# Kernel optimization log

Measured on AMD Instinct MI355X. Metric: run time of the kernel, lower is better.

The kernel has to match this reference:

```python
import jax, jax.numpy as jnp
import numpy as np

FP4_E2M1_VALUES = [0.0, 0.0625, 8.0, 1.0, 2.0, 3.0, 4.0, 6.0,
                   -0.0, -0.0625, -8.0, -1.0, -2.0, -3.0, -4.0, -6.0]

M, N, K = 4096, 4096, 4096


def setup_inputs() -> dict:
    key = jax.random.key(0)
    k1, k2 = jax.random.split(key)
    x = jax.random.normal(k1, (M, K), dtype=jnp.float16)
    # packed uint8 bytes stored as int32 (values in [0,256)); each byte holds
    # two fp4 indices: high nibble = even k, low nibble = odd k
    packed_weight = jax.random.randint(k2, (N, K // 2), 0, 256, dtype=jnp.int32)
    lut = jnp.array(FP4_E2M1_VALUES, dtype=jnp.float16)
    return {"x": x, "packed_weight": packed_weight, "lut": lut}


def reference(x, packed_weight, lut):
    # Dequantize: unpack nibbles along K, LUT lookup -> W [N, K] fp16
    n, kh = packed_weight.shape
    high = (packed_weight >> 4) & 15   # even k positions
    low = packed_weight & 15           # odd k positions
    idx = jnp.stack([high, low], axis=-1).reshape(n, 2 * kh)  # [N, K]
    w = lut[idx]                       # [N, K] fp16
    # GEMM with fp32 accumulation (Triton kernel accumulates in fp32), cast to fp16
    y = jnp.einsum('mk,nk->mn', x, w, preferred_element_type=jnp.float32)
    return y.astype(jnp.float16)
```

## Files before the change

### kernel.cpp

```cpp
#include <hip/hip_runtime.h>
#include <hip/hip_fp16.h>
#include <stdint.h>

#define M_DIM 4096
#define N_DIM 4096
#define K_DIM 4096
#define KW (K_DIM / 2)
#define WS_XH_BYTES ((size_t)M_DIM * K_DIM * 2)
#define WS_WH_BYTES ((size_t)N_DIM * K_DIM * 2)

typedef _Float16 half8 __attribute__((ext_vector_type(8)));
typedef float f32x4 __attribute__((ext_vector_type(4)));

__device__ __forceinline__ uint32_t pk2(float a, float b) {
  auto h = __builtin_amdgcn_cvt_pkrtz(a, b);
  return __builtin_bit_cast(uint32_t, h);
}

__device__ __forceinline__ uint32_t dq(uint32_t b, uint32_t ph, uint32_t pl) {
#if __has_builtin(__builtin_amdgcn_perm)
  const uint32_t sel = ((b & 0x70u) << 4) | ((b & 0x07u) << 24);
  uint32_t v = __builtin_amdgcn_perm(ph, pl, sel);
#else
  const uint64_t pool = ((uint64_t)ph << 32) | pl;
  const uint32_t mh = (uint32_t)(pool >> (((b >> 4) & 7u) * 8)) & 0xFFu;
  const uint32_t ml = (uint32_t)(pool >> ((b & 7u) * 8)) & 0xFFu;
  uint32_t v = (mh << 8) | (ml << 24);
#endif
  const uint32_t sg = ((b & 0x88u) * 0x10000100u) & 0x80008000u;
  return v | sg;
}

__device__ __forceinline__ void lut_pool(const float* __restrict__ lutf,
                                         uint32_t& ph, uint32_t& pl) {
  const uint32_t h01 = pk2(lutf[0], lutf[1]);
  const uint32_t h23 = pk2(lutf[2], lutf[3]);
  const uint32_t h45 = pk2(lutf[4], lutf[5]);
  const uint32_t h67 = pk2(lutf[6], lutf[7]);
#if __has_builtin(__builtin_amdgcn_perm)
  pl = __builtin_amdgcn_perm(h23, h01, 0x07050301u);
  ph = __builtin_amdgcn_perm(h67, h45, 0x07050301u);
#else
  pl = ((h01 >> 8) & 0xFFu) | ((h01 >> 24) << 8) |
       (((h23 >> 8) & 0xFFu) << 16) | ((h23 >> 24) << 24);
  ph = ((h45 >> 8) & 0xFFu) | ((h45 >> 24) << 8) |
       (((h67 >> 8) & 0xFFu) << 16) | ((h67 >> 24) << 24);
#endif
}

#define XBLOCKS (M_DIM * K_DIM / 8 / 256)
#define WBLOCKS (N_DIM * KW / 4 / 256)

__global__ __launch_bounds__(256) void prep_kernel(
    const float4* __restrict__ xin, uint4* __restrict__ xout,
    const int4* __restrict__ pin, uint4* __restrict__ wout,
    const float* __restrict__ lutf) {
  const int b = blockIdx.x;
  if (b < XBLOCKS) {
    const int i = b * 256 + threadIdx.x;
    const float4 v0 = xin[2 * i];
    const float4 v1 = xin[2 * i + 1];
    xout[i] = make_uint4(pk2(v0.x, v0.y), pk2(v0.z, v0.w),
                         pk2(v1.x, v1.y), pk2(v1.z, v1.w));
  } else {
    uint32_t ph, pl;
    lut_pool(lutf, ph, pl);
    const int i = (b - XBLOCKS) * 256 + threadIdx.x;
    const int4 w = pin[i];
    wout[i] = make_uint4(dq(w.x, ph, pl), dq(w.y, ph, pl),
                         dq(w.z, ph, pl), dq(w.w, ph, pl));
  }
}

__global__ __launch_bounds__(256) void cvt_x_kernel(const float4* __restrict__ xin,
                                                    uint4* __restrict__ xout) {
  const int i = blockIdx.x * 256 + threadIdx.x;
  const float4 v0 = xin[2 * i];
  const float4 v1 = xin[2 * i + 1];
  xout[i] = make_uint4(pk2(v0.x, v0.y), pk2(v0.z, v0.w),
                       pk2(v1.x, v1.y), pk2(v1.z, v1.w));
}

__device__ __forceinline__ f32x4 mfma16(half8 a, half8 b, f32x4 c) {
  return __builtin_amdgcn_mfma_f32_16x16x32_f16(a, b, c, 0, 0, 0);
}

#define NT (K_DIM / 64)
#define SGB __builtin_amdgcn_sched_group_barrier
#define SG_MFMA 0x8
#define SG_VMEM 0x10
#define SG_DSRD 0x100

__global__ __launch_bounds__(512, 2) void f16gemm256_kernel(
    const uint8_t* __restrict__ xh,
    const uint8_t* __restrict__ wh,
    float* __restrict__ out)
{
  __shared__ uint16_t Al[2][2][256 * 32];
  __shared__ uint16_t Bl[2][2][256 * 32];

  const int tid  = threadIdx.x;
  const int lane = tid & 63;
  const int wave = tid >> 6;
  const int wm   = wave >> 2;
  const int wn   = wave & 3;

  const int bid = blockIdx.x;
  const int sw  = (bid & 7) * 32 + (bid >> 3);
  const int m0  = (sw >> 4) * 256;
  const int n0  = (sw & 15) * 256;

  const uint8_t* asrc[2];
  const uint8_t* bsrc[2];
  int ldst[2];
#pragma unroll
  for (int s = 0; s < 2; ++s) {
    const int slot = tid + s * 512;
    const int row  = slot >> 2;
    const int g    = (slot & 3) ^ ((row >> 1) & 3);
    asrc[s] = xh + ((size_t)(m0 + row) * K_DIM) * 2 + g * 16;
    bsrc[s] = wh + ((size_t)(n0 + row) * K_DIM) * 2 + g * 16;
    ldst[s] = slot * 16;
  }

  auto STAGE = [&](int isB, int buf, int kh, int tt) {
    const int koff  = tt * 128 + kh * 64;
    uint8_t* lb = (uint8_t*)(isB ? &Bl[0][0][0] : &Al[0][0][0]) +
                  (buf * 2 + kh) * 16384;
#pragma unroll
    for (int s = 0; s < 2; ++s) {
      const uint8_t* gp = (isB ? bsrc[s] : asrc[s]) + koff;
      __builtin_amdgcn_global_load_lds(
          (const __attribute__((address_space(1))) uint32_t*)gp,
          (__attribute__((address_space(3))) uint32_t*)(lb + ldst[s]), 16, 0, 0);
    }
  };

  int aoff[8], boff[4];
#pragma unroll
  for (int m = 0; m < 8; ++m) {
    const int row = wm * 128 + m * 16 + (lane & 15);
    const int ch  = (lane >> 4) ^ ((row >> 1) & 3);
    aoff[m] = row * 32 + ch * 8;
  }
#pragma unroll
  for (int n = 0; n < 4; ++n) {
    const int row = wn * 64 + n * 16 + (lane & 15);
    const int ch  = (lane >> 4) ^ ((row >> 1) & 3);
    boff[n] = row * 32 + ch * 8;
  }

  f32x4 acc[8][4];
#pragma unroll
  for (int i = 0; i < 8; ++i)
#pragma unroll
    for (int j = 0; j < 4; ++j) acc[i][j] = (f32x4){0.f, 0.f, 0.f, 0.f};

  STAGE(1, 0, 0, 0);
  STAGE(0, 0, 0, 0);
  STAGE(1, 0, 1, 0);
  STAGE(0, 0, 1, 0);
  asm volatile("s_waitcnt vmcnt(0)" ::: "memory");
  __builtin_amdgcn_s_barrier();

  half8 af[8], bfr[4];

#pragma unroll 2
  for (int t = 0; t < NT; ++t) {
    const int cur = t & 1;
    const uint16_t* Ab = &Al[cur][0][0];
    const uint16_t* Bb = &Bl[cur][0][0];
    const bool st1 = (t + 1 < NT);

    __builtin_amdgcn_s_setprio(1);

    bfr[0] = *(const half8*)(Bb + boff[0]);
    bfr[1] = *(const half8*)(Bb + boff[1]);
    bfr[2] = *(const half8*)(Bb + boff[2]);
    bfr[3] = *(const half8*)(Bb + boff[3]);
    af[0] = *(const half8*)(Ab + aoff[0]);
    af[1] = *(const half8*)(Ab + aoff[1]);

    if (st1) {
      STAGE(1, cur ^ 1, 0, t + 1);
      STAGE(0, cur ^ 1, 0, t + 1);
      STAGE(1, cur ^ 1, 1, t + 1);
      STAGE(0, cur ^ 1, 1, t + 1);
    }

#pragma unroll
    for (int m = 2; m < 8; ++m) af[m] = *(const half8*)(Ab + aoff[m]);

#pragma unroll
    for (int m = 0; m < 8; ++m) {
      acc[m][0] = mfma16(af[m], bfr[0], acc[m][0]);
      acc[m][1] = mfma16(af[m], bfr[1], acc[m][1]);
      acc[m][2] = mfma16(af[m], bfr[2], acc[m][2]);
      acc[m][3] = mfma16(af[m], bfr[3], acc[m][3]);
    }

    bfr[0] = *(const half8*)(Bb + 8192 + boff[0]);
    bfr[1] = *(const half8*)(Bb + 8192 + boff[1]);
    bfr[2] = *(const half8*)(Bb + 8192 + boff[2]);
    bfr[3] = *(const half8*)(Bb + 8192 + boff[3]);
#pragma unroll
    for (int m = 0; m < 8; ++m) af[m] = *(const half8*)(Ab + 8192 + aoff[m]);

#pragma unroll
    for (int m = 0; m < 8; ++m) {
      acc[m][0] = mfma16(af[m], bfr[0], acc[m][0]);
      acc[m][1] = mfma16(af[m], bfr[1], acc[m][1]);
      acc[m][2] = mfma16(af[m], bfr[2], acc[m][2]);
      acc[m][3] = mfma16(af[m], bfr[3], acc[m][3]);
    }

    SGB(SG_DSRD, 6, 0);
    SGB(SG_VMEM, 8, 0);
#pragma unroll
    for (int i = 0; i < 18; ++i) {
      SGB(SG_MFMA, 2, 0);
      SGB(SG_DSRD, 1, 0);
    }
    SGB(SG_MFMA, 28, 0);

    __builtin_amdgcn_s_setprio(0);
    if (st1) asm volatile("s_waitcnt vmcnt(0)" ::: "memory");
    __builtin_amdgcn_s_barrier();
  }

  const int mb = m0 + wm * 128 + (lane >> 4) * 4;
  const int nb = n0 + wn * 64 + (lane & 15);
#pragma unroll
  for (int m = 0; m < 8; ++m)
#pragma unroll
    for (int n = 0; n < 4; ++n)
#pragma unroll
      for (int r = 0; r < 4; ++r)
        out[(size_t)(mb + m * 16 + r) * N_DIM + (nb + n * 16)] = acc[m][n][r];
}

#define BM 128
#define BN 128
#define BK 32

__global__ __launch_bounds__(256, 2) void fp4gemm_kernel(
    const uint8_t* __restrict__ xh, const int* __restrict__ pw,
    const float* __restrict__ lutf, float* __restrict__ out)
{
  __shared__ uint16_t ldsA[BM * BK];
  __shared__ uint16_t ldsB[BN * BK];

  const int tid  = threadIdx.x;
  const int lane = tid & 63;
  const int wave = tid >> 6;
  const int wm   = wave >> 1;
  const int wn   = wave & 1;
  const int m0 = blockIdx.y * BM;
  const int n0 = blockIdx.x * BN;

  uint32_t ph, pl;
  lut_pool(lutf, ph, pl);

  f32x4 acc[4][4];
#pragma unroll
  for (int i = 0; i < 4; ++i)
#pragma unroll
    for (int j = 0; j < 4; ++j) acc[i][j] = (f32x4){0.f, 0.f, 0.f, 0.f};

  const int rowB  = tid >> 1;
  const int halfB = tid & 1;
  const int swzB  = (rowB >> 1) & 3;

  for (int kt = 0; kt < K_DIM / BK; ++kt) {
    __syncthreads();

#pragma unroll
    for (int s = 0; s < 2; ++s) {
      const int idx = tid + s * 256;
      const int row = idx >> 2;
      const int c16 = idx & 3;
      const int g16 = c16 ^ ((row >> 1) & 3);
      const uint8_t* gp = xh + ((size_t)(m0 + row) * K_DIM + kt * BK) * 2 + g16 * 16;
      uint8_t* lp = (uint8_t*)ldsA + (size_t)idx * 16;
      __builtin_amdgcn_global_load_lds(
          (const __attribute__((address_space(1))) uint32_t*)gp,
          (__attribute__((address_space(3))) uint32_t*)lp, 16, 0, 0);
    }

    {
      const int* gp = pw + (size_t)(n0 + rowB) * KW + kt * (BK / 2) + halfB * 8;
      const int4 wA = ((const int4*)gp)[0];
      const int4 wB = ((const int4*)gp)[1];
      uint8_t* base = (uint8_t*)ldsB + rowB * 64;
      *(uint4*)(base + ((halfB * 2 + 0) ^ swzB) * 16) =
          make_uint4(dq(wA.x, ph, pl), dq(wA.y, ph, pl),
                     dq(wA.z, ph, pl), dq(wA.w, ph, pl));
      *(uint4*)(base + ((halfB * 2 + 1) ^ swzB) * 16) =
          make_uint4(dq(wB.x, ph, pl), dq(wB.y, ph, pl),
                     dq(wB.z, ph, pl), dq(wB.w, ph, pl));
    }

    __syncthreads();

    const int q = lane >> 4;
    half8 af[4], bfr[4];
#pragma unroll
    for (int i = 0; i < 4; ++i) {
      const int row = wm * 64 + i * 16 + (lane & 15);
      af[i] = *(const half8*)(ldsA + row * BK + (q ^ ((row >> 1) & 3)) * 8);
    }
#pragma unroll
    for (int j = 0; j < 4; ++j) {
      const int row = wn * 64 + j * 16 + (lane & 15);
      bfr[j] = *(const half8*)(ldsB + row * BK + (q ^ ((row >> 1) & 3)) * 8);
    }
#pragma unroll
    for (int i = 0; i < 4; ++i)
#pragma unroll
      for (int j = 0; j < 4; ++j)
        acc[i][j] = __builtin_amdgcn_mfma_f32_16x16x32_f16(af[i], bfr[j], acc[i][j], 0, 0, 0);
  }

  const int mb = m0 + wm * 64 + (lane >> 4) * 4;
  const int nb = n0 + wn * 64 + (lane & 15);
#pragma unroll
  for (int i = 0; i < 4; ++i)
#pragma unroll
    for (int j = 0; j < 4; ++j)
#pragma unroll
      for (int r = 0; r < 4; ++r)
        out[(size_t)(mb + i * 16 + r) * N_DIM + (nb + j * 16)] = acc[i][j][r];
}

extern "C" void kernel_launch(void* const* d_in, const int* in_sizes, int n_in,
                              void* d_out, int out_size, void* d_ws, size_t ws_size,
                              hipStream_t stream) {
  const void* px = nullptr; const void* ppw = nullptr; const void* plut = nullptr;
  for (int i = 0; i < n_in; ++i) {
    const long s = in_sizes[i];
    if (s == (long)M_DIM * K_DIM) px = d_in[i];
    else if (s == (long)N_DIM * KW) ppw = d_in[i];
    else if (s == 16) plut = d_in[i];
  }
  if (!px || !ppw || !plut) { px = d_in[0]; ppw = d_in[1]; plut = d_in[2]; }

  if (ws_size >= WS_XH_BYTES + WS_WH_BYTES) {
    uint8_t* wh = (uint8_t*)d_ws + WS_XH_BYTES;
    prep_kernel<<<XBLOCKS + WBLOCKS, 256, 0, stream>>>(
        (const float4*)px, (uint4*)d_ws, (const int4*)ppw, (uint4*)wh,
        (const float*)plut);
    f16gemm256_kernel<<<dim3(256), dim3(512), 0, stream>>>(
        (const uint8_t*)d_ws, wh, (float*)d_out);
  } else {
    cvt_x_kernel<<<(M_DIM * K_DIM / 8) / 256, 256, 0, stream>>>(
        (const float4*)px, (uint4*)d_ws);
    dim3 grid(N_DIM / BN, M_DIM / BM);
    fp4gemm_kernel<<<grid, dim3(256), 0, stream>>>(
        (const uint8_t*)d_ws, (const int*)ppw, (const float*)plut, (float*)d_out);
  }
}
```

Before: 258.9 us.

## Load A fragments directly from global into registers, stage only B in LDS

The kernel stops staging the activation tile in shared memory. Each wave now loads its A fragments straight from global memory into registers, interleaved with the MFMAs, and only B goes through LDS via a finer-grained half-tile pipeline with partial vmcnt waits. The aim is to halve LDS traffic and LDS footprint, cut LDS read instructions, and possibly allow better occupancy. The cost is that A loads are no longer shared between the four waves in each wave row, so global and L2 traffic for A rises. Latency hiding now depends on vmcnt counts, and there are two barriers per iteration instead of one.

```diff
diff --git a/kernel.cpp b/kernel.cpp
--- a/kernel.cpp
+++ b/kernel.cpp
@@ -96,7 +96,6 @@
     const uint8_t* __restrict__ wh,
     float* __restrict__ out)
 {
-  __shared__ uint16_t Al[2][2][256 * 32];
   __shared__ uint16_t Bl[2][2][256 * 32];
 
   const int tid  = threadIdx.x;
@@ -110,7 +109,6 @@
   const int m0  = (sw >> 4) * 256;
   const int n0  = (sw & 15) * 256;
 
-  const uint8_t* asrc[2];
   const uint8_t* bsrc[2];
   int ldst[2];
 #pragma unroll
@@ -118,31 +116,22 @@
     const int slot = tid + s * 512;
     const int row  = slot >> 2;
     const int g    = (slot & 3) ^ ((row >> 1) & 3);
-    asrc[s] = xh + ((size_t)(m0 + row) * K_DIM) * 2 + g * 16;
     bsrc[s] = wh + ((size_t)(n0 + row) * K_DIM) * 2 + g * 16;
     ldst[s] = slot * 16;
   }
 
-  auto STAGE = [&](int isB, int buf, int kh, int tt) {
+  auto STAGEB = [&](int buf, int kh, int tt) {
     const int koff  = tt * 128 + kh * 64;
-    uint8_t* lb = (uint8_t*)(isB ? &Bl[0][0][0] : &Al[0][0][0]) +
-                  (buf * 2 + kh) * 16384;
+    uint8_t* lb = (uint8_t*)&Bl[0][0][0] + (buf * 2 + kh) * 16384;
 #pragma unroll
     for (int s = 0; s < 2; ++s) {
-      const uint8_t* gp = (isB ? bsrc[s] : asrc[s]) + koff;
       __builtin_amdgcn_global_load_lds(
-          (const __attribute__((address_space(1))) uint32_t*)gp,
+          (const __attribute__((address_space(1))) uint32_t*)(bsrc[s] + koff),
           (__attribute__((address_space(3))) uint32_t*)(lb + ldst[s]), 16, 0, 0);
     }
   };
 
-  int aoff[8], boff[4];
-#pragma unroll
-  for (int m = 0; m < 8; ++m) {
-    const int row = wm * 128 + m * 16 + (lane & 15);
-    const int ch  = (lane >> 4) ^ ((row >> 1) & 3);
-    aoff[m] = row * 32 + ch * 8;
-  }
+  int boff[4];
 #pragma unroll
   for (int n = 0; n < 4; ++n) {
     const int row = wn * 64 + n * 16 + (lane & 15);
@@ -150,81 +139,76 @@
     boff[n] = row * 32 + ch * 8;
   }
 
+  const uint8_t* Ax = xh + (size_t)(m0 + wm * 128 + (lane & 15)) * (K_DIM * 2)
+                         + (lane >> 4) * 16;
+
   f32x4 acc[8][4];
 #pragma unroll
   for (int i = 0; i < 8; ++i)
 #pragma unroll
     for (int j = 0; j < 4; ++j) acc[i][j] = (f32x4){0.f, 0.f, 0.f, 0.f};
 
-  STAGE(1, 0, 0, 0);
-  STAGE(0, 0, 0, 0);
-  STAGE(1, 0, 1, 0);
-  STAGE(0, 0, 1, 0);
-  asm volatile("s_waitcnt vmcnt(0)" ::: "memory");
+  half8 af[8], bfr[4];
+
+  STAGEB(0, 0, 0);
+  STAGEB(0, 1, 0);
+  STAGEB(1, 0, 1);
+#pragma unroll
+  for (int m = 0; m < 8; ++m)
+    af[m] = *(const half8*)(Ax + m * (16 * K_DIM * 2));
+  asm volatile("s_waitcnt vmcnt(12)" ::: "memory");
   __builtin_amdgcn_s_barrier();
-
-  half8 af[8], bfr[4];
 
 #pragma unroll 2
   for (int t = 0; t < NT; ++t) {
     const int cur = t & 1;
-    const uint16_t* Ab = &Al[cur][0][0];
     const uint16_t* Bb = &Bl[cur][0][0];
     const bool st1 = (t + 1 < NT);
+    const bool st2 = (t + 2 < NT);
 
     __builtin_amdgcn_s_setprio(1);
-
     bfr[0] = *(const half8*)(Bb + boff[0]);
     bfr[1] = *(const half8*)(Bb + boff[1]);
     bfr[2] = *(const half8*)(Bb + boff[2]);
     bfr[3] = *(const half8*)(Bb + boff[3]);
-    af[0] = *(const half8*)(Ab + aoff[0]);
-    af[1] = *(const half8*)(Ab + aoff[1]);
-
-    if (st1) {
-      STAGE(1, cur ^ 1, 0, t + 1);
-      STAGE(0, cur ^ 1, 0, t + 1);
-      STAGE(1, cur ^ 1, 1, t + 1);
-      STAGE(0, cur ^ 1, 1, t + 1);
-    }
-
-#pragma unroll
-    for (int m = 2; m < 8; ++m) af[m] = *(const half8*)(Ab + aoff[m]);
-
+    if (st1) STAGEB(cur ^ 1, 1, t + 1);
 #pragma unroll
     for (int m = 0; m < 8; ++m) {
       acc[m][0] = mfma16(af[m], bfr[0], acc[m][0]);
       acc[m][1] = mfma16(af[m], bfr[1], acc[m][1]);
       acc[m][2] = mfma16(af[m], bfr[2], acc[m][2]);
       acc[m][3] = mfma16(af[m], bfr[3], acc[m][3]);
-    }
-
+      af[m] = *(const half8*)(Ax + m * (16 * K_DIM * 2) + t * 128 + 64);
+    }
+    SGB(SG_DSRD, 4, 0);
+    SGB(SG_VMEM, 2, 0);
+#pragma unroll
+    for (int i = 0; i < 8; ++i) { SGB(SG_MFMA, 4, 0); SGB(SG_VMEM, 1, 0); }
+    __builtin_amdgcn_s_setprio(0);
+    asm volatile("s_waitcnt vmcnt(10)" ::: "memory");
+    __builtin_amdgcn_s_barrier();
+
+    __builtin_amdgcn_s_setprio(1);
     bfr[0] = *(const half8*)(Bb + 8192 + boff[0]);
     bfr[1] = *(const half8*)(Bb + 8192 + boff[1]);
     bfr[2] = *(const half8*)(Bb + 8192 + boff[2]);
     bfr[3] = *(const half8*)(Bb + 8192 + boff[3]);
-#pragma unroll
-    for (int m = 0; m < 8; ++m) af[m] = *(const half8*)(Ab + 8192 + aoff[m]);
-
+    if (st2) STAGEB(cur, 0, t + 2);
 #pragma unroll
     for (int m = 0; m < 8; ++m) {
       acc[m][0] = mfma16(af[m], bfr[0], acc[m][0]);
       acc[m][1] = mfma16(af[m], bfr[1], acc[m][1]);
       acc[m][2] = mfma16(af[m], bfr[2], acc[m][2]);
       acc[m][3] = mfma16(af[m], bfr[3], acc[m][3]);
-    }
-
-    SGB(SG_DSRD, 6, 0);
-    SGB(SG_VMEM, 8, 0);
-#pragma unroll
-    for (int i = 0; i < 18; ++i) {
-      SGB(SG_MFMA, 2, 0);
-      SGB(SG_DSRD, 1, 0);
-    }
-    SGB(SG_MFMA, 28, 0);
-
+      if (st1)
+        af[m] = *(const half8*)(Ax + m * (16 * K_DIM * 2) + (t + 1) * 128);
+    }
+    SGB(SG_DSRD, 4, 0);
+    SGB(SG_VMEM, 2, 0);
+#pragma unroll
+    for (int i = 0; i < 8; ++i) { SGB(SG_MFMA, 4, 0); SGB(SG_VMEM, 1, 0); }
     __builtin_amdgcn_s_setprio(0);
-    if (st1) asm volatile("s_waitcnt vmcnt(0)" ::: "memory");
+    asm volatile("s_waitcnt vmcnt(10)" ::: "memory");
     __builtin_amdgcn_s_barrier();
   }
 
```

After: 485.3 us. 1.87x slower.
